# Performance work log

Hardware: AMD Instinct MI355X
Metric: run time of the kernel (lower is better)

The kernel has to match this reference:

```python
import jax, jax.numpy as jnp
import numpy as np

EPS = 1e-5


def setup_inputs() -> dict:
    key = jax.random.key(0)
    ks = jax.random.split(key, 7)
    B, T, H = 4, 4096, 1024
    x = jax.random.normal(ks[0], (B, T, H), dtype=jnp.float32)
    gamma = jnp.ones((H,), dtype=jnp.float32)
    beta = jnp.zeros((H,), dtype=jnp.float32)
    s = 1.0 / np.sqrt(H)
    Wg = jax.random.uniform(ks[1], (H, H), minval=-s, maxval=s, dtype=jnp.float32)
    bg = jax.random.uniform(ks[2], (H,), minval=-s, maxval=s, dtype=jnp.float32)
    Wc = jax.random.uniform(ks[3], (H, H), minval=-s, maxval=s, dtype=jnp.float32)
    bc = jax.random.uniform(ks[4], (H,), minval=-s, maxval=s, dtype=jnp.float32)
    return {"x": x, "gamma": gamma, "beta": beta, "Wg": Wg, "bg": bg, "Wc": Wc, "bc": bc}


def reference(x, gamma, beta, Wg, bg, Wc, bc):
    # x: [B, T, H]
    mu = jnp.mean(x, axis=-1, keepdims=True)
    var = jnp.mean((x - mu) ** 2, axis=-1, keepdims=True)
    normed = (x - mu) * jax.lax.rsqrt(var + EPS) * gamma + beta
    z = jax.nn.sigmoid(jnp.einsum('bth,oh->bto', normed, Wg) + bg)  # gate
    c = jnp.einsum('bth,oh->bto', normed, Wc) + bc                  # candidate
    B, T, H = x.shape

    def step(h, zc):
        z_t, c_t = zc  # each [B, H]
        h = (1.0 - z_t) * h + z_t * c_t
        return h, h

    h0 = jnp.zeros((B, H), dtype=x.dtype)
    # scan over time: move T to leading axis
    _, hs = jax.lax.scan(step, h0, (jnp.swapaxes(z, 0, 1), jnp.swapaxes(c, 0, 1)))
    return jnp.swapaxes(hs, 0, 1) + x  # residual
```

## Files before the change

kernel.cpp:

```cpp
#include <hip/hip_runtime.h>
#include <stdint.h>


#define B_    4
#define T_    4096
#define H_    1024
#define BT_   (B_*T_)
#define EPSV  1e-5f
#define CHK   256
#define CL    (T_/CHK)
#define NG    16
#define BM    256
#define BN    128
#define BK    32

typedef float  f32x4  __attribute__((ext_vector_type(4)));
typedef __bf16 bf16x8 __attribute__((ext_vector_type(8)));
typedef unsigned short u16;

#define ASM_VMCNT(N) asm volatile("s_waitcnt vmcnt(" #N ")" ::: "memory")
#define ASM_BAR()    asm volatile("s_barrier" ::: "memory")

__device__ __forceinline__ u16 f2bf(float f) {
  uint32_t u = __builtin_bit_cast(uint32_t, f);
  u += 0x7fffu + ((u >> 16) & 1u);
  return (u16)(u >> 16);
}
__device__ __forceinline__ float bf2f(uint32_t u) {
  uint32_t v = (u & 0xffffu) << 16;
  return __builtin_bit_cast(float, v);
}
__device__ __forceinline__ void bf4(uint2 p, float* f) {
  f[0] = bf2f(p.x); f[1] = bf2f(p.x >> 16);
  f[2] = bf2f(p.y); f[3] = bf2f(p.y >> 16);
}

__global__ __launch_bounds__(256) void ln_kernel(
    const float* __restrict__ x, const float* __restrict__ gamma,
    const float* __restrict__ beta, u16* __restrict__ normed) {
  const int wid  = threadIdx.x >> 6, lane = threadIdx.x & 63;
  const int row  = blockIdx.x * 4 + wid;
  const float4* xr = reinterpret_cast<const float4*>(x + (size_t)row * H_);
  float4 v[4];
  float s = 0.0f, q = 0.0f;
  #pragma unroll
  for (int seg = 0; seg < 4; ++seg) {
    v[seg] = xr[seg * 64 + lane];
    s += v[seg].x + v[seg].y + v[seg].z + v[seg].w;
    q += v[seg].x*v[seg].x + v[seg].y*v[seg].y + v[seg].z*v[seg].z + v[seg].w*v[seg].w;
  }
  #pragma unroll
  for (int off = 1; off < 64; off <<= 1) {
    s += __shfl_xor(s, off);
    q += __shfl_xor(q, off);
  }
  const float mean = s * (1.0f / H_);
  const float var  = q * (1.0f / H_) - mean * mean;
  const float rstd = rsqrtf(var + EPSV);
  const float4* g4 = reinterpret_cast<const float4*>(gamma);
  const float4* b4 = reinterpret_cast<const float4*>(beta);
  uint2* o2 = reinterpret_cast<uint2*>(normed + (size_t)row * H_);
  #pragma unroll
  for (int seg = 0; seg < 4; ++seg) {
    const float4 g = g4[seg * 64 + lane];
    const float4 b = b4[seg * 64 + lane];
    uint2 o;
    o.x = (uint32_t)f2bf((v[seg].x - mean) * rstd * g.x + b.x)
        | ((uint32_t)f2bf((v[seg].y - mean) * rstd * g.y + b.y) << 16);
    o.y = (uint32_t)f2bf((v[seg].z - mean) * rstd * g.z + b.z)
        | ((uint32_t)f2bf((v[seg].w - mean) * rstd * g.w + b.w) << 16);
    o2[seg * 64 + lane] = o;
  }
}

__global__ __launch_bounds__(256) void pack_kernel(
    const float* __restrict__ Wg, const float* __restrict__ Wc,
    u16* __restrict__ wpack) {
  const int idx4 = (blockIdx.x * 256 + threadIdx.x) * 4;
  const int n = idx4 >> 10;
  const int k = idx4 & 1023;
  const float* src = (n < 1024) ? (Wg + (size_t)n * 1024 + k)
                                : (Wc + (size_t)(n - 1024) * 1024 + k);
  const float4 v = *reinterpret_cast<const float4*>(src);
  uint2 o;
  o.x = (uint32_t)f2bf(v.x) | ((uint32_t)f2bf(v.y) << 16);
  o.y = (uint32_t)f2bf(v.z) | ((uint32_t)f2bf(v.w) << 16);
  *reinterpret_cast<uint2*>(wpack + idx4) = o;
}

__global__ __launch_bounds__(256, 2) void gemm_kernel(
    const u16* __restrict__ A, const u16* __restrict__ Bw,
    const float* __restrict__ bg, const float* __restrict__ bc,
    u16* __restrict__ zbuf, u16* __restrict__ cbuf) {
  __shared__ u16 As[3][BM * BK];
  __shared__ u16 Bs[3][BN * BK];
  const int bid = blockIdx.x;
  const int nb  = (bid & 7) * 128 + (bid >> 3);
  const int mt  = nb >> 4, nt = nb & 15;
  const int tid = threadIdx.x;
  const int wid = tid >> 6, lane = tid & 63;
  const int wr  = wid >> 1, wcq = wid & 1;
  const int frow = lane & 15;
  const int physslot = (lane >> 4) ^ ((frow >> 1) & 3);

  f32x4 acc[8][4] = {};

  const u16* aptr[4];
  const u16* bptr[2];
  #pragma unroll
  for (int i = 0; i < 4; ++i) {
    const int c = tid + 256 * i;
    const int row = c >> 2;
    const int sl = (c & 3) ^ ((row >> 1) & 3);
    aptr[i] = A + (size_t)(mt * BM + row) * 1024 + sl * 8;
  }
  #pragma unroll
  for (int i = 0; i < 2; ++i) {
    const int c = tid + 256 * i;
    const int row = c >> 2;
    const int sl = (c & 3) ^ ((row >> 1) & 3);
    bptr[i] = Bw + (size_t)(nt * BN + row) * 1024 + sl * 8;
  }

  auto stage = [&](int buf, int ks) {
    const int kk = ks * BK;
    #pragma unroll
    for (int i = 0; i < 4; ++i)
      __builtin_amdgcn_global_load_lds(
          (const __attribute__((address_space(1))) void*)(aptr[i] + kk),
          (__attribute__((address_space(3))) void*)&As[buf][(tid + 256 * i) * 8], 16, 0, 0);
    #pragma unroll
    for (int i = 0; i < 2; ++i)
      __builtin_amdgcn_global_load_lds(
          (const __attribute__((address_space(1))) void*)(bptr[i] + kk),
          (__attribute__((address_space(3))) void*)&Bs[buf][(tid + 256 * i) * 8], 16, 0, 0);
  };
  auto compute = [&](int buf) {
    bf16x8 bfr[4];
    #pragma unroll
    for (int n = 0; n < 4; ++n)
      bfr[n] = *reinterpret_cast<const bf16x8*>(
          &Bs[buf][(wcq * 64 + n * 16 + frow) * BK + physslot * 8]);
    __builtin_amdgcn_s_setprio(1);
    #pragma unroll
    for (int m = 0; m < 8; ++m) {
      const bf16x8 am = *reinterpret_cast<const bf16x8*>(
          &As[buf][(wr * 128 + m * 16 + frow) * BK + physslot * 8]);
      #pragma unroll
      for (int n = 0; n < 4; ++n)
        acc[m][n] = __builtin_amdgcn_mfma_f32_16x16x32_bf16(am, bfr[n], acc[m][n], 0, 0, 0);
    }
    __builtin_amdgcn_s_setprio(0);
  };

  stage(0, 0);
  stage(1, 1);
  for (int ks = 0; ks < 30; ++ks) {
    ASM_VMCNT(6);
    ASM_BAR();
    stage((ks + 2) % 3, ks + 2);
    compute(ks % 3);
  }
  ASM_VMCNT(6);  ASM_BAR();
  compute(0);
  ASM_VMCNT(0);  ASM_BAR();
  compute(1);

  const int r0 = (lane >> 4) * 4;
  const int col16 = lane & 15;
  const bool isz = (nt < 8);
  #pragma unroll
  for (int m = 0; m < 8; ++m) {
    #pragma unroll
    for (int n = 0; n < 4; ++n) {
      const int col = nt * BN + wcq * 64 + n * 16 + col16;
      #pragma unroll
      for (int r = 0; r < 4; ++r) {
        const int row = mt * BM + wr * 128 + m * 16 + r0 + r;
        float v = acc[m][n][r];
        if (isz) {
          v += bg[col];
          v = 1.0f / (1.0f + __expf(-v));
          zbuf[(size_t)row * 1024 + col] = f2bf(v);
        } else {
          const int cc = col - 1024;
          v += bc[cc];
          cbuf[(size_t)row * 1024 + cc] = f2bf(v);
        }
      }
    }
  }
}

__global__ __launch_bounds__(256) void scan1_kernel(
    const u16* __restrict__ zbuf, const u16* __restrict__ cbuf,
    float* __restrict__ Achk, float* __restrict__ Uchk) {
  const int bid   = blockIdx.x;
  const int chunk = bid & (CHK - 1);
  const int b     = bid >> 8;
  const int o4    = threadIdx.x * 4;
  const size_t base = ((size_t)(b * T_ + chunk * CL)) * H_ + o4;
  float A[4] = {1.f, 1.f, 1.f, 1.f};
  float u[4] = {0.f, 0.f, 0.f, 0.f};
  #pragma unroll
  for (int t = 0; t < CL; ++t) {
    const size_t idx = base + (size_t)t * H_;
    const uint2 zp = *reinterpret_cast<const uint2*>(&zbuf[idx]);
    const uint2 cp = *reinterpret_cast<const uint2*>(&cbuf[idx]);
    float z[4], c[4];
    bf4(zp, z); bf4(cp, c);
    #pragma unroll
    for (int j = 0; j < 4; ++j) {
      const float a = 1.0f - z[j];
      A[j] *= a;
      u[j] = a * u[j] + z[j] * c[j];
    }
  }
  const int idx = (b * CHK + chunk) * H_ + o4;
  *reinterpret_cast<float4*>(&Achk[idx]) = make_float4(A[0], A[1], A[2], A[3]);
  *reinterpret_cast<float4*>(&Uchk[idx]) = make_float4(u[0], u[1], u[2], u[3]);
}

__global__ __launch_bounds__(256) void scan2ab_kernel(
    const float* __restrict__ Achk, const float* __restrict__ Uchk,
    float* __restrict__ Hgrp) {
  const int t    = blockIdx.x * 256 + threadIdx.x;
  const int b    = t >> 14;
  const int idx  = t & 16383;
  const int o    = idx >> 4;
  const int g    = idx & 15;
  const int lane = threadIdx.x & 63;

  float A = 1.0f, u = 0.0f;
  #pragma unroll
  for (int c = 0; c < 16; ++c) {
    const int chunk = g * 16 + c;
    const int e = (b * CHK + chunk) * H_ + o;
    const float a = Achk[e];
    u = a * u + Uchk[e];
    A *= a;
  }
  #pragma unroll
  for (int d = 1; d < 16; d <<= 1) {
    const float Ap = __shfl_up(A, d, 16);
    const float up = __shfl_up(u, d, 16);
    if ((lane & 15) >= d) {
      u = A * up + u;
      A = A * Ap;
    }
  }
  const float hg = __shfl_up(u, 1, 16);
  Hgrp[(b * NG + g) * H_ + o] = (g == 0) ? 0.0f : hg;
}

__global__ __launch_bounds__(256) void scan3_kernel(
    const u16* __restrict__ zbuf, const u16* __restrict__ cbuf,
    const float* __restrict__ Achk, const float* __restrict__ Uchk,
    const float* __restrict__ Hgrp, const float* __restrict__ x,
    float* __restrict__ out) {
  const int bid   = blockIdx.x;
  const int chunk = bid & (CHK - 1);
  const int b     = bid >> 8;
  const int g     = chunk >> 4;
  const int o4    = threadIdx.x * 4;

  float4 hv = *reinterpret_cast<const float4*>(&Hgrp[(b * NG + g) * H_ + o4]);
  float h[4] = {hv.x, hv.y, hv.z, hv.w};
  for (int jc = g * 16; jc < chunk; ++jc) {
    const int e = (b * CHK + jc) * H_ + o4;
    const float4 a4 = *reinterpret_cast<const float4*>(&Achk[e]);
    const float4 u4 = *reinterpret_cast<const float4*>(&Uchk[e]);
    h[0] = a4.x * h[0] + u4.x;
    h[1] = a4.y * h[1] + u4.y;
    h[2] = a4.z * h[2] + u4.z;
    h[3] = a4.w * h[3] + u4.w;
  }

  const size_t base = ((size_t)(b * T_ + chunk * CL)) * H_ + o4;
  #pragma unroll
  for (int t = 0; t < CL; ++t) {
    const size_t idx = base + (size_t)t * H_;
    const uint2 zp = *reinterpret_cast<const uint2*>(&zbuf[idx]);
    const uint2 cp = *reinterpret_cast<const uint2*>(&cbuf[idx]);
    const float4 xv = *reinterpret_cast<const float4*>(&x[idx]);
    float z[4], c[4];
    bf4(zp, z); bf4(cp, c);
    #pragma unroll
    for (int j = 0; j < 4; ++j)
      h[j] = (1.0f - z[j]) * h[j] + z[j] * c[j];
    *reinterpret_cast<float4*>(&out[idx]) =
        make_float4(h[0] + xv.x, h[1] + xv.y, h[2] + xv.z, h[3] + xv.w);
  }
}

extern "C" void kernel_launch(void* const* d_in, const int* in_sizes, int n_in,
                              void* d_out, int out_size, void* d_ws, size_t ws_size,
                              hipStream_t stream) {
  const float* x     = (const float*)d_in[0];
  const float* gamma = (const float*)d_in[1];
  const float* beta  = (const float*)d_in[2];
  const float* Wg    = (const float*)d_in[3];
  const float* bg    = (const float*)d_in[4];
  const float* Wc    = (const float*)d_in[5];
  const float* bc    = (const float*)d_in[6];
  float* out = (float*)d_out;

  char* ws = (char*)d_ws;
  u16*   normed = (u16*)(ws);
  u16*   wpack  = (u16*)(ws + 33554432ull);
  u16*   zbuf   = (u16*)(ws + 37748736ull);
  u16*   cbuf   = (u16*)(ws + 71303168ull);
  float* Achk   = (float*)(ws);
  float* Uchk   = (float*)(ws + 4194304ull);
  float* Hgrp   = (float*)(ws + 8388608ull);

  ln_kernel  <<<BT_/4, 256, 0, stream>>>(x, gamma, beta, normed);
  pack_kernel<<<2048,  256, 0, stream>>>(Wg, Wc, wpack);
  gemm_kernel<<<1024,  256, 0, stream>>>(normed, wpack, bg, bc, zbuf, cbuf);
  scan1_kernel <<<B_*CHK, 256, 0, stream>>>(zbuf, cbuf, Achk, Uchk);
  scan2ab_kernel<<<(B_*H_*NG)/256, 256, 0, stream>>>(Achk, Uchk, Hgrp);
  scan3_kernel <<<B_*CHK, 256, 0, stream>>>(zbuf, cbuf, Achk, Uchk, Hgrp, x, out);
}
```

Baseline: 299.1 us.

## Enlarge GEMM tile to 256x256 with BK=64 and 512-thread blocks

Restructures the bf16 GEMM from 256x128 tiles with BK=32 and triple buffering to 256x256 tiles with BK=64, double buffering and 8 waves per block. The B-tile load is interleaved into the compute loop to overlap with the MFMAs, and the LDS swizzle is adapted to 64-wide rows. Larger tiles raise arithmetic intensity and halve the number of k-iterations and barriers. In exchange the pipeline is shallower, LDS use per block is higher, and only 512 blocks are launched, which may reduce occupancy or latency hiding.

```diff
diff --git a/kernel.cpp b/kernel.cpp
--- a/kernel.cpp
+++ b/kernel.cpp
@@ -10,9 +10,7 @@
 #define CHK   256
 #define CL    (T_/CHK)
 #define NG    16
-#define BM    256
-#define BN    128
-#define BK    32
+#define KT    16
 
 typedef float  f32x4  __attribute__((ext_vector_type(4)));
 typedef __bf16 bf16x8 __attribute__((ext_vector_type(8)));
@@ -88,95 +86,115 @@
   *reinterpret_cast<uint2*>(wpack + idx4) = o;
 }
 
-__global__ __launch_bounds__(256, 2) void gemm_kernel(
+__global__ __launch_bounds__(512, 2) void gemm_kernel(
     const u16* __restrict__ A, const u16* __restrict__ Bw,
     const float* __restrict__ bg, const float* __restrict__ bc,
     u16* __restrict__ zbuf, u16* __restrict__ cbuf) {
-  __shared__ u16 As[3][BM * BK];
-  __shared__ u16 Bs[3][BN * BK];
+  __shared__ u16 As[2][2][128 * 64];
+  __shared__ u16 Bs[2][2][128 * 64];
   const int bid = blockIdx.x;
-  const int nb  = (bid & 7) * 128 + (bid >> 3);
-  const int mt  = nb >> 4, nt = nb & 15;
+  const int nb  = (bid & 7) * 64 + (bid >> 3);
+  const int mt  = nb >> 3, nt = nb & 7;
   const int tid = threadIdx.x;
   const int wid = tid >> 6, lane = tid & 63;
-  const int wr  = wid >> 1, wcq = wid & 1;
-  const int frow = lane & 15;
-  const int physslot = (lane >> 4) ^ ((frow >> 1) & 3);
+  const int wr  = wid >> 2, wc = wid & 3;
+  const int frow = lane & 15, hi = lane >> 4;
 
   f32x4 acc[8][4] = {};
 
-  const u16* aptr[4];
-  const u16* bptr[2];
-  #pragma unroll
-  for (int i = 0; i < 4; ++i) {
-    const int c = tid + 256 * i;
-    const int row = c >> 2;
-    const int sl = (c & 3) ^ ((row >> 1) & 3);
-    aptr[i] = A + (size_t)(mt * BM + row) * 1024 + sl * 8;
-  }
+  const u16* aS[2][2];
+  const u16* bS[2][2];
   #pragma unroll
   for (int i = 0; i < 2; ++i) {
-    const int c = tid + 256 * i;
-    const int row = c >> 2;
-    const int sl = (c & 3) ^ ((row >> 1) & 3);
-    bptr[i] = Bw + (size_t)(nt * BN + row) * 1024 + sl * 8;
-  }
-
-  auto stage = [&](int buf, int ks) {
-    const int kk = ks * BK;
-    #pragma unroll
-    for (int i = 0; i < 4; ++i)
-      __builtin_amdgcn_global_load_lds(
-          (const __attribute__((address_space(1))) void*)(aptr[i] + kk),
-          (__attribute__((address_space(3))) void*)&As[buf][(tid + 256 * i) * 8], 16, 0, 0);
-    #pragma unroll
-    for (int i = 0; i < 2; ++i)
-      __builtin_amdgcn_global_load_lds(
-          (const __attribute__((address_space(1))) void*)(bptr[i] + kk),
-          (__attribute__((address_space(3))) void*)&Bs[buf][(tid + 256 * i) * 8], 16, 0, 0);
+    const int c  = tid + i * 512;
+    const int r  = c >> 3;
+    const int sl = (c & 7) ^ (r & 7);
+    #pragma unroll
+    for (int h = 0; h < 2; ++h) {
+      aS[h][i] = A  + (size_t)(mt * 256 + h * 128 + r) * 1024 + sl * 8;
+      bS[h][i] = Bw + (size_t)(nt * 256 + h * 128 + r) * 1024 + sl * 8;
+    }
+  }
+
+  auto stageA = [&](int buf, int t) {
+    const int ko = t * 64;
+    #pragma unroll
+    for (int h = 0; h < 2; ++h)
+      #pragma unroll
+      for (int i = 0; i < 2; ++i)
+        __builtin_amdgcn_global_load_lds(
+            (const __attribute__((address_space(1))) void*)(aS[h][i] + ko),
+            (__attribute__((address_space(3))) void*)&As[buf][h][(tid + i * 512) * 8],
+            16, 0, 0);
   };
-  auto compute = [&](int buf) {
-    bf16x8 bfr[4];
+  auto stageB = [&](int buf, int t) {
+    const int ko = t * 64;
+    #pragma unroll
+    for (int h = 0; h < 2; ++h)
+      #pragma unroll
+      for (int i = 0; i < 2; ++i)
+        __builtin_amdgcn_global_load_lds(
+            (const __attribute__((address_space(1))) void*)(bS[h][i] + ko),
+            (__attribute__((address_space(3))) void*)&Bs[buf][h][(tid + i * 512) * 8],
+            16, 0, 0);
+  };
+
+  stageA(0, 0);
+  stageB(0, 0);
+  for (int t = 0; t < KT; ++t) {
+    const int cb = t & 1;
+    if (t < KT - 1) { stageA(cb ^ 1, t + 1); ASM_VMCNT(4); }
+    else            { ASM_VMCNT(0); }
+    ASM_BAR();
+
+    bf16x8 bfr[4][2];
     #pragma unroll
     for (int n = 0; n < 4; ++n)
-      bfr[n] = *reinterpret_cast<const bf16x8*>(
-          &Bs[buf][(wcq * 64 + n * 16 + frow) * BK + physslot * 8]);
-    __builtin_amdgcn_s_setprio(1);
-    #pragma unroll
-    for (int m = 0; m < 8; ++m) {
-      const bf16x8 am = *reinterpret_cast<const bf16x8*>(
-          &As[buf][(wr * 128 + m * 16 + frow) * BK + physslot * 8]);
-      #pragma unroll
-      for (int n = 0; n < 4; ++n)
-        acc[m][n] = __builtin_amdgcn_mfma_f32_16x16x32_bf16(am, bfr[n], acc[m][n], 0, 0, 0);
-    }
-    __builtin_amdgcn_s_setprio(0);
-  };
-
-  stage(0, 0);
-  stage(1, 1);
-  for (int ks = 0; ks < 30; ++ks) {
-    ASM_VMCNT(6);
+      #pragma unroll
+      for (int kk = 0; kk < 2; ++kk) {
+        const int cl = wc * 64 + n * 16 + frow;
+        const int bh = cl >> 7, lr = cl & 127;
+        const int ps = (kk * 4 + hi) ^ (lr & 7);
+        bfr[n][kk] = *reinterpret_cast<const bf16x8*>(&Bs[cb][bh][lr * 64 + ps * 8]);
+      }
+
+    #pragma unroll
+    for (int p = 0; p < 4; ++p) {
+      if (p == 1 && t < KT - 1) stageB(cb ^ 1, t + 1);
+      bf16x8 af[2][2];
+      #pragma unroll
+      for (int mm = 0; mm < 2; ++mm)
+        #pragma unroll
+        for (int kk = 0; kk < 2; ++kk) {
+          const int lr = (p * 2 + mm) * 16 + frow;
+          const int ps = (kk * 4 + hi) ^ (lr & 7);
+          af[mm][kk] = *reinterpret_cast<const bf16x8*>(&As[cb][wr][lr * 64 + ps * 8]);
+        }
+      __builtin_amdgcn_s_setprio(1);
+      #pragma unroll
+      for (int mm = 0; mm < 2; ++mm)
+        #pragma unroll
+        for (int n = 0; n < 4; ++n)
+          #pragma unroll
+          for (int kk = 0; kk < 2; ++kk)
+            acc[p * 2 + mm][n] = __builtin_amdgcn_mfma_f32_16x16x32_bf16(
+                af[mm][kk], bfr[n][kk], acc[p * 2 + mm][n], 0, 0, 0);
+      __builtin_amdgcn_s_setprio(0);
+    }
     ASM_BAR();
-    stage((ks + 2) % 3, ks + 2);
-    compute(ks % 3);
-  }
-  ASM_VMCNT(6);  ASM_BAR();
-  compute(0);
-  ASM_VMCNT(0);  ASM_BAR();
-  compute(1);
-
-  const int r0 = (lane >> 4) * 4;
-  const int col16 = lane & 15;
-  const bool isz = (nt < 8);
+  }
+
+  const int r0 = hi * 4;
+  const int col16 = frow;
+  const bool isz = (nt < 4);
   #pragma unroll
   for (int m = 0; m < 8; ++m) {
     #pragma unroll
     for (int n = 0; n < 4; ++n) {
-      const int col = nt * BN + wcq * 64 + n * 16 + col16;
+      const int col = nt * 256 + wc * 64 + n * 16 + col16;
       #pragma unroll
       for (int r = 0; r < 4; ++r) {
-        const int row = mt * BM + wr * 128 + m * 16 + r0 + r;
+        const int row = mt * 256 + wr * 128 + m * 16 + r0 + r;
         float v = acc[m][n][r];
         if (isz) {
           v += bg[col];
@@ -316,7 +334,7 @@
 
   ln_kernel  <<<BT_/4, 256, 0, stream>>>(x, gamma, beta, normed);
   pack_kernel<<<2048,  256, 0, stream>>>(Wg, Wc, wpack);
-  gemm_kernel<<<1024,  256, 0, stream>>>(normed, wpack, bg, bc, zbuf, cbuf);
+  gemm_kernel<<<512,   512, 0, stream>>>(normed, wpack, bg, bc, zbuf, cbuf);
   scan1_kernel <<<B_*CHK, 256, 0, stream>>>(zbuf, cbuf, Achk, Uchk);
   scan2ab_kernel<<<(B_*H_*NG)/256, 256, 0, stream>>>(Achk, Uchk, Hgrp);
   scan3_kernel <<<B_*CHK, 256, 0, stream>>>(zbuf, cbuf, Achk, Uchk, Hgrp, x, out);
```

Measured after the change: 293.6 us. About the same (-1.8%).
